# Kernel optimization log

Measured on AMD Instinct MI355X. Metric: run time of the kernel, lower is better.

The kernel has to match this reference:

```python
import jax, jax.numpy as jnp
import numpy as np

D, NH, K, FF, S, B = 256, 4, 1024, 1024, 2048, 4  # nhead*d_model must equal key_feature_dim=1024


def _ln(x, g, b, eps=1e-5):
    m = jnp.mean(x, axis=-1, keepdims=True)
    v = jnp.mean((x - m) ** 2, axis=-1, keepdims=True)
    return (x - m) / jnp.sqrt(v + eps) * g + b


def _l2norm(x, eps=1e-12):  # F.normalize(p=2, dim=-1)
    n = jnp.sqrt(jnp.sum(x * x, axis=-1, keepdims=True))
    return x / jnp.maximum(n, eps)


def setup_inputs() -> dict:
    key = jax.random.key(0)
    ks = jax.random.split(key, 16)
    def rn(i, shape, s):
        return jax.random.normal(ks[i], shape, jnp.float32) * jnp.float32(s)
    z = lambda shape: jnp.zeros(shape, jnp.float32)
    o = lambda shape: jnp.ones(shape, jnp.float32)
    return {
        "srcc": jax.random.normal(ks[0], (S, B, D), jnp.float32),
        "memory": jax.random.normal(ks[1], (S, B, D), jnp.float32),
        # per-head RelationUnit weights (stacked over NH heads)
        "WK": rn(2, (NH, K, D), np.sqrt(2.0 / K)),
        "WQ": rn(3, (NH, K, D), np.sqrt(2.0 / K)),
        "WV": rn(4, (NH, D, D), np.sqrt(2.0 / D)),
        "Wt": rn(5, (NH, D, D), np.sqrt(1.0 / D)),   # trans_conv
        # per-head TransNonlinear (extra_nonlinear)
        "e1w": rn(6, (NH, K, D), np.sqrt(1.0 / D)), "e1b": z((NH, K)),
        "e2w": rn(7, (NH, D, K), np.sqrt(1.0 / K)), "e2b": z((NH, D)),
        "eg": o((NH, D)), "eb": z((NH, D)),
        "Wout": rn(8, (D, NH * D), np.sqrt(1.0 / (NH * D))),  # trans_conv_out
        # decoder-layer FFN + norms
        "l1w": rn(9, (FF, D), np.sqrt(1.0 / D)), "l1b": z((FF,)),
        "l2w": rn(10, (D, FF), np.sqrt(1.0 / FF)), "l2b": z((D,)),
        "n1g": o((D,)), "n1b": z((D,)),
        "n3g": o((D,)), "n3b": z((D,)),
    }


def _forward(srcc, memory, WK, WQ, WV, Wt, e1w, e1b, e2w, e2b, eg, eb,
             Wout, l1w, l1b, l2w, l2b, n1g, n1b, n3g, n3b):
    # RMA(query=memory, key=srcc, value=srcc); dropout = identity (eval mode)
    q, kv = memory, srcc  # [S,B,D]
    wk = _l2norm(jnp.einsum('sbd,hkd->hsbk', kv, WK))   # [h,S,B,K]
    wq = _l2norm(jnp.einsum('sbd,hkd->hsbk', q, WQ))
    dot = jnp.einsum('hqbk,hsbk->hbqs', wq, wk)          # [h,B,Sq,Sk]
    aff = jax.nn.softmax(dot, axis=-1)
    # custom renormalization over the *query* axis (torch dim=1 of [B,Sq,Sk])
    aff = aff / (1e-9 + jnp.sum(aff, axis=2, keepdims=True))
    wv = jnp.einsum('sbd,hed->hbse', kv, WV)             # [h,B,Sk,D]
    o = jnp.einsum('hbqs,hbse->hqbe', aff, wv)           # [h,Sq,B,D]
    ru = jax.nn.relu(jnp.einsum('hqbd,hed->hqbe', q[None] - o, Wt))
    # per-head TransNonlinear
    hmid = jax.nn.relu(jnp.einsum('hqbd,hkd->hqbk', ru, e1w) + e1b[:, None, None, :])
    s2 = jnp.einsum('hqbk,hdk->hqbd', hmid, e2w) + e2b[:, None, None, :]
    xh = _ln(ru + s2, eg[:, None, None, :], eb[:, None, None, :])  # [h,S,B,D]
    cat = jnp.moveaxis(xh, 0, 2).reshape(q.shape[0], q.shape[1], NH * D)  # concat heads
    rma_out = jnp.einsum('sbk,dk->sbd', cat, Wout)       # [S,B,D]
    # decoder layer: note the faithful `[0]` indexing from the source
    srcc2 = rma_out[0]                                    # [B,D]
    x = _ln(memory + srcc2[None, :, :], n1g, n1b)         # broadcast residual
    ff = jax.nn.relu(x @ l1w.T + l1b) @ l2w.T + l2b
    return _ln(x + ff, n3g, n3b)


def reference(srcc, memory, WK, WQ, WV, Wt, e1w, e1b, e2w, e2b, eg, eb,
              Wout, l1w, l1b, l2w, l2b, n1g, n1b, n3g, n3b):
    return _forward(srcc, memory, WK, WQ, WV, Wt, e1w, e1b, e2w, e2b, eg, eb,
                    Wout, l1w, l1b, l2w, l2b, n1g, n1b, n3g, n3b)
```

## Files before the change

### kernel.cpp

```cpp
#include <hip/hip_runtime.h>
#include <stdint.h>
#include <stdio.h>

#define S_  2048
#define B_  4
#define D_  256
#define NH_ 4
#define K_  1024
#define FF_ 1024
#define M_  (S_*B_)
#define HB_ (NH_*B_)

#define LDSROW 136
#define PROW 144

typedef float  f32x4  __attribute__((ext_vector_type(4)));
typedef __bf16 bf16x8 __attribute__((ext_vector_type(8)));

__device__ __forceinline__ float bf2f(unsigned short u) {
  union { unsigned int i; float f; } v; v.i = ((unsigned int)u) << 16; return v.f;
}
__device__ __forceinline__ unsigned short f2bf(float f) {
  union { float f; unsigned int i; } v; v.f = f;
  unsigned int r = v.i + 0x7fffu + ((v.i >> 16) & 1u);
  return (unsigned short)(r >> 16);
}
__device__ __forceinline__ unsigned char f2fp8(float f) {
  return (unsigned char)(__builtin_amdgcn_cvt_pk_fp8_f32(f, f, 0, false) & 0xff);
}

__device__ __forceinline__ void gld_lds16(const void* g, void* l) {
  __builtin_amdgcn_global_load_lds(
      (__attribute__((address_space(1))) void*)(uintptr_t)g,
      (__attribute__((address_space(3))) void*)(uintptr_t)l, 16, 0, 0);
}

__device__ __forceinline__ void gemm_kloop(
    const unsigned short* __restrict__ Ag, const unsigned short* __restrict__ Bg,
    int lda, int ldb, int kdim,
    unsigned short* __restrict__ smA, unsigned short* __restrict__ smB,
    f32x4 acc[4][4])
{
  const int t    = threadIdx.x;
  const int wave = t >> 6;
  const int lane = t & 63;
  const int wm   = (wave >> 1) << 6;
  const int wn   = (wave & 1) << 6;
  const int c16  = lane & 15;
  const int quad = lane >> 4;

  for (int kc = 0; kc < kdim; kc += 64) {
    __syncthreads();
#pragma unroll
    for (int it = 0; it < 4; ++it) {
      int c   = it*256 + t;
      int row = c >> 3;
      int g   = (c & 7) ^ (row & 7);
      const unsigned short* ga = Ag + (size_t)row*lda + kc + g*8;
      const unsigned short* gb = Bg + (size_t)row*ldb + kc + g*8;
      unsigned short* la = smA + (size_t)(it*256 + wave*64)*8;
      unsigned short* lb = smB + (size_t)(it*256 + wave*64)*8;
      gld_lds16(ga, la);
      gld_lds16(gb, lb);
    }
    asm volatile("s_waitcnt vmcnt(0)" ::: "memory");
    __syncthreads();
#pragma unroll
    for (int ks = 0; ks < 2; ++ks) {
      bf16x8 av[4], bv[4];
#pragma unroll
      for (int i = 0; i < 4; ++i) {
        int ra = wm + i*16 + c16;
        av[i] = *(const bf16x8*)(smA + ra*64 + (((ks*4 + quad) ^ (ra & 7)))*8);
        int rb = wn + i*16 + c16;
        bv[i] = *(const bf16x8*)(smB + rb*64 + (((ks*4 + quad) ^ (rb & 7)))*8);
      }
#pragma unroll
      for (int i = 0; i < 4; ++i)
#pragma unroll
        for (int j = 0; j < 4; ++j)
          acc[i][j] = __builtin_amdgcn_mfma_f32_16x16x32_bf16(av[i], bv[j], acc[i][j], 0, 0, 0);
    }
  }
}

__device__ __forceinline__ float blk_sum256(float v, float* red) {
#pragma unroll
  for (int o = 32; o; o >>= 1) v += __shfl_xor(v, o, 64);
  __syncthreads();
  if ((threadIdx.x & 63) == 0) red[threadIdx.x >> 6] = v;
  __syncthreads();
  return red[0] + red[1] + red[2] + red[3];
}

__device__ __forceinline__ float wave_red(float a) {
#pragma unroll
  for (int o = 1; o < 64; o <<= 1) a += __shfl_xor(a, o, 64);
  return a;
}

__global__ void __launch_bounds__(256) k_cvt6(
    const float* __restrict__ s0, unsigned short* __restrict__ d0,
    const float* __restrict__ s1, unsigned short* __restrict__ d1,
    const float* __restrict__ s2, unsigned short* __restrict__ d2,
    const float* __restrict__ s3, unsigned short* __restrict__ d3,
    const float* __restrict__ s4, unsigned short* __restrict__ d4,
    const float* __restrict__ s5, unsigned short* __restrict__ d5) {
  int b = blockIdx.x;
  const float* src; unsigned short* dst; int base;
  if      (b < 2048) { src = s0; dst = d0; base = b; }
  else if (b < 4096) { src = s1; dst = d1; base = b - 2048; }
  else if (b < 5120) { src = s2; dst = d2; base = b - 4096; }
  else if (b < 6144) { src = s3; dst = d3; base = b - 5120; }
  else if (b < 6400) { src = s4; dst = d4; base = b - 6144; }
  else               { src = s5; dst = d5; base = b - 6400; }
  int i = (base*256 + threadIdx.x)*4;
  float4 v = *(const float4*)(src + i);
  ushort4 o;
  o.x = f2bf(v.x); o.y = f2bf(v.y); o.z = f2bf(v.z); o.w = f2bf(v.w);
  *(ushort4*)(dst + i) = o;
}

__global__ void __launch_bounds__(256) k_proj(const unsigned short* __restrict__ X,
    const unsigned short* __restrict__ W, float* __restrict__ nsq,
    unsigned char* __restrict__ outp) {
  __shared__ __align__(16) unsigned short sm[128*LDSROW];
  int l = blockIdx.x, x = l & 7, rblk = l >> 3;
  int m0 = (rblk >> 2)*128;
  int n0 = (x*4 + (rblk & 3))*128;
  f32x4 acc[4][4];
#pragma unroll
  for (int i = 0; i < 4; ++i)
#pragma unroll
    for (int j = 0; j < 4; ++j) acc[i][j] = f32x4{0.f,0.f,0.f,0.f};
  gemm_kloop(X + (size_t)m0*D_, W + (size_t)n0*D_, D_, D_, D_, sm, sm + 128*64, acc);
  const int t = threadIdx.x, wave = t>>6, lane = t&63;
  const int wm = (wave>>1)*64, wn = (wave&1)*64, quad = lane>>4, c16 = lane&15;
  const int h = n0 >> 10;
  unsigned char* sm8 = (unsigned char*)sm;
  __syncthreads();
#pragma unroll
  for (int i = 0; i < 4; ++i)
#pragma unroll
    for (int r = 0; r < 4; ++r) {
      int mloc = wm + i*16 + quad*4 + r;
      float sq = 0.f;
#pragma unroll
      for (int j = 0; j < 4; ++j) {
        float v = acc[i][j][r];
        sm8[mloc*PROW + wn + j*16 + c16] = f2fp8(v);
        sq += v*v;
      }
      sq += __shfl_xor(sq, 1, 64); sq += __shfl_xor(sq, 2, 64);
      sq += __shfl_xor(sq, 4, 64); sq += __shfl_xor(sq, 8, 64);
      if (c16 == 0) {
        int m = m0 + mloc;
        atomicAdd(&nsq[(size_t)(h*B_ + (m & 3))*S_ + (m >> 2)], sq);
      }
    }
  __syncthreads();
  const int cg = t & 7, rsub = t >> 3;
#pragma unroll
  for (int c = 0; c < 4; ++c) {
    int mloc = c*32 + rsub;
    int m = m0 + mloc, s = m >> 2, b = m & 3;
    uint4 val = *(const uint4*)(sm8 + mloc*PROW + cg*16);
    *(uint4*)(outp + ((size_t)(h*B_ + b)*S_ + s)*K_ + (n0 & (K_-1)) + cg*16) = val;
  }
}

__global__ void __launch_bounds__(256) k_qkA(const unsigned char* __restrict__ wqa,
    const unsigned char* __restrict__ wka, const float* __restrict__ nq,
    const float* __restrict__ nk, float* __restrict__ lrow,
    unsigned short* __restrict__ E) {
  __shared__ __align__(16) unsigned short sm[128*LDSROW];
  unsigned char* smA = (unsigned char*)sm;
  unsigned char* smB = smA + 128*128;
  int l = blockIdx.x, x = l & 7, rblk = l >> 3;
  int hb = rblk >> 5;
  int rr = rblk & 31;
  int q0 = (x*2 + (rr & 1))*128;
  int s0 = (rr >> 1)*128;
  const unsigned char* A  = wqa + (size_t)hb*S_*K_ + (size_t)q0*K_;
  const unsigned char* Bm = wka + (size_t)hb*S_*K_ + (size_t)s0*K_;
  const int t = threadIdx.x, wave = t>>6, lane = t&63;
  const int wm = (wave>>1)*64, wn = (wave&1)*64, quad = lane>>4, c16 = lane&15;
  f32x4 acc[4][4];
#pragma unroll
  for (int i = 0; i < 4; ++i)
#pragma unroll
    for (int j = 0; j < 4; ++j) acc[i][j] = f32x4{0.f,0.f,0.f,0.f};

  for (int kc = 0; kc < K_; kc += 128) {
    __syncthreads();
#pragma unroll
    for (int it = 0; it < 4; ++it) {
      int c   = it*256 + t;
      int row = c >> 3;
      int g   = (c & 7) ^ (row & 7);
      gld_lds16(A  + (size_t)row*K_ + kc + g*16, smA + (size_t)(it*256 + wave*64)*16);
      gld_lds16(Bm + (size_t)row*K_ + kc + g*16, smB + (size_t)(it*256 + wave*64)*16);
    }
    asm volatile("s_waitcnt vmcnt(0)" ::: "memory");
    __syncthreads();
#pragma unroll
    for (int ks = 0; ks < 4; ++ks) {
      long av[4], bv[4];
#pragma unroll
      for (int i = 0; i < 4; ++i) {
        int ra = wm + i*16 + c16;
        av[i] = *(const long*)(smA + ra*128 + (((2*ks + (quad>>1)) ^ (ra & 7)))*16 + (quad&1)*8);
        int rb = wn + i*16 + c16;
        bv[i] = *(const long*)(smB + rb*128 + (((2*ks + (quad>>1)) ^ (rb & 7)))*16 + (quad&1)*8);
      }
#pragma unroll
      for (int i = 0; i < 4; ++i)
#pragma unroll
        for (int j = 0; j < 4; ++j)
          acc[i][j] = __builtin_amdgcn_mfma_f32_16x16x32_fp8_fp8(av[i], bv[j], acc[i][j], 0, 0, 0);
    }
  }

  float rk4[4];
#pragma unroll
  for (int j = 0; j < 4; ++j)
    rk4[j] = rsqrtf(nk[(size_t)hb*S_ + s0 + wn + j*16 + c16]);
  __syncthreads();
#pragma unroll
  for (int i = 0; i < 4; ++i)
#pragma unroll
    for (int r = 0; r < 4; ++r) {
      int qloc = wm + i*16 + quad*4 + r;
      float rq = rsqrtf(nq[(size_t)hb*S_ + q0 + qloc]);
      float rs = 0.f;
#pragma unroll
      for (int j = 0; j < 4; ++j) {
        float e = __expf(acc[i][j][r] * rq * rk4[j]);
        rs += e;
        sm[qloc*LDSROW + wn + j*16 + c16] = f2bf(e);
      }
      rs += __shfl_xor(rs, 1, 64); rs += __shfl_xor(rs, 2, 64);
      rs += __shfl_xor(rs, 4, 64); rs += __shfl_xor(rs, 8, 64);
      if (c16 == 0) atomicAdd(&lrow[(size_t)hb*S_ + q0 + qloc], rs);
    }
  __syncthreads();
  const int col8 = (t & 15)*8, rsub = t >> 4;
#pragma unroll
  for (int c = 0; c < 8; ++c) {
    int qloc = c*16 + rsub;
    uint4 val = *(const uint4*)(sm + qloc*LDSROW + col8);
    *(uint4*)(E + ((size_t)hb*S_ + q0 + qloc)*S_ + s0 + col8) = val;
  }
}

__global__ void __launch_bounds__(256) k_colsumE(const unsigned short* __restrict__ E,
    const float* __restrict__ lrow, float* __restrict__ colsum,
    float* __restrict__ p0) {
  __shared__ float il[128];
  int hb = blockIdx.x, qc = blockIdx.y;
  int t  = threadIdx.x;
  if (t < 128) il[t] = 1.f / lrow[(size_t)hb*S_ + qc*128 + t];
  __syncthreads();
  const unsigned short* Eb = E + (size_t)hb*S_*S_ + (size_t)(qc*128)*S_ + t*8;
  float acc8[8] = {0,0,0,0,0,0,0,0};
  for (int qi = 0; qi < 128; ++qi) {
    uint4 u = *(const uint4*)(Eb + (size_t)qi*S_);
    float w = il[qi];
    unsigned int ws_[4] = {u.x, u.y, u.z, u.w};
    float v8[8];
#pragma unroll
    for (int k = 0; k < 4; ++k) {
      v8[2*k]   = bf2f((unsigned short)(ws_[k] & 0xffffu));
      v8[2*k+1] = bf2f((unsigned short)(ws_[k] >> 16));
    }
#pragma unroll
    for (int k = 0; k < 8; ++k) acc8[k] += v8[k] * w;
    if (qc == 0 && qi == 0) {
#pragma unroll
      for (int k = 0; k < 8; ++k) p0[(size_t)hb*S_ + t*8 + k] = v8[k] * w;
    }
  }
#pragma unroll
  for (int k = 0; k < 8; ++k)
    atomicAdd(&colsum[(size_t)hb*S_ + t*8 + k], acc8[k]);
}

__global__ void __launch_bounds__(256) k_mid0(const float* __restrict__ p0,
    const float* __restrict__ colsum, const float* __restrict__ kv,
    float* __restrict__ cbuf) {
  __shared__ float aff[128];
  int hb = blockIdx.x, sc = blockIdx.y;
  int b = hb & 3;
  int t = threadIdx.x;
  if (t < 128) {
    int s = sc*128 + t;
    aff[t] = p0[(size_t)hb*S_ + s] / (1e-9f + colsum[(size_t)hb*S_ + s]);
  }
  __syncthreads();
  float acc = 0.f;
#pragma unroll 4
  for (int i = 0; i < 128; ++i) {
    int s = sc*128 + i;
    acc += aff[i] * kv[((size_t)s*B_ + b)*D_ + t];
  }
  atomicAdd(&cbuf[hb*D_ + t], acc);
}

__global__ void __launch_bounds__(256) k_mid1a(const float* __restrict__ cbuf,
    const float* __restrict__ mem, const float* __restrict__ WV,
    const float* __restrict__ Wt, float* __restrict__ ruW) {
  __shared__ float cS[D_], qmo[D_];
  int hb = blockIdx.x, h = hb >> 2, b = hb & 3;
  int t = threadIdx.x, wave = t >> 6, lane = t & 63;
  cS[t] = cbuf[hb*D_ + t];
  __syncthreads();
  float4 cv = *(const float4*)(cS + lane*4);
  for (int rr = 0; rr < 64; ++rr) {
    int e = wave*64 + rr;
    float4 w = *(const float4*)(WV + ((size_t)h*D_ + e)*D_ + lane*4);
    float a = wave_red(cv.x*w.x + cv.y*w.y + cv.z*w.z + cv.w*w.w);
    if (lane == 0) qmo[e] = mem[(size_t)b*D_ + e] - a;
  }
  __syncthreads();
  float4 qv = *(const float4*)(qmo + lane*4);
  for (int rr = 0; rr < 64; ++rr) {
    int e = wave*64 + rr;
    float4 w = *(const float4*)(Wt + ((size_t)h*D_ + e)*D_ + lane*4);
    float a = wave_red(qv.x*w.x + qv.y*w.y + qv.z*w.z + qv.w*w.w);
    if (lane == 0) ruW[hb*D_ + e] = fmaxf(a, 0.f);
  }
}

__global__ void __launch_bounds__(256) k_mid1b(const float* __restrict__ ruW,
    const float* __restrict__ e1w, const float* __restrict__ e1b,
    float* __restrict__ hmW) {
  __shared__ float ru[D_];
  int hb = blockIdx.x, kc = blockIdx.y, h = hb >> 2;
  int t = threadIdx.x, wave = t >> 6, lane = t & 63;
  ru[t] = ruW[hb*D_ + t];
  __syncthreads();
  float4 rv = *(const float4*)(ru + lane*4);
  for (int rr = 0; rr < 32; ++rr) {
    int k = kc*128 + wave*32 + rr;
    float4 w = *(const float4*)(e1w + ((size_t)h*K_ + k)*D_ + lane*4);
    float a = wave_red(rv.x*w.x + rv.y*w.y + rv.z*w.z + rv.w*w.w);
    if (lane == 0) hmW[hb*K_ + k] = fmaxf(a + e1b[(size_t)h*K_ + k], 0.f);
  }
}

__global__ void __launch_bounds__(256) k_mid1c(const float* __restrict__ hmW,
    const float* __restrict__ e2w, const float* __restrict__ e2b,
    float* __restrict__ s2W) {
  __shared__ float hm[K_];
  int hb = blockIdx.x, dc = blockIdx.y, h = hb >> 2;
  int t = threadIdx.x, wave = t >> 6, lane = t & 63;
  for (int k = t; k < K_; k += 256) hm[k] = hmW[hb*K_ + k];
  __syncthreads();
  for (int rr = 0; rr < 32; ++rr) {
    int d = dc*128 + wave*32 + rr;
    const float* row = e2w + ((size_t)h*D_ + d)*K_;
    float a = 0.f;
#pragma unroll
    for (int p = 0; p < 4; ++p) {
      float4 w = *(const float4*)(row + (p*64 + lane)*4);
      float4 hv = *(const float4*)(hm + (p*64 + lane)*4);
      a += w.x*hv.x + w.y*hv.y + w.z*hv.z + w.w*hv.w;
    }
    a = wave_red(a);
    if (lane == 0) s2W[hb*D_ + d] = a + e2b[(size_t)h*D_ + d];
  }
}

__global__ void __launch_bounds__(256) k_mid1d(const float* __restrict__ ruW,
    const float* __restrict__ s2W, const float* __restrict__ eg,
    const float* __restrict__ ebias, float* __restrict__ xh0) {
  __shared__ float red[4];
  int hb = blockIdx.x, h = hb >> 2;
  int t = threadIdx.x;
  float tv = ruW[hb*D_ + t] + s2W[hb*D_ + t];
  float mean = blk_sum256(tv, red) * (1.f/D_);
  float dv = tv - mean;
  float var = blk_sum256(dv*dv, red) * (1.f/D_);
  xh0[hb*D_ + t] = dv * rsqrtf(var + 1e-5f) * eg[(size_t)h*D_ + t] + ebias[(size_t)h*D_ + t];
}

__global__ void __launch_bounds__(256) k_mid2(const float* __restrict__ xh0,
    const float* __restrict__ Wout, float* __restrict__ srcc2) {
  __shared__ float cat[NH_*D_];
  int b = blockIdx.x, dc = blockIdx.y;
  int t = threadIdx.x, wave = t >> 6, lane = t & 63;
  for (int n = t; n < NH_*D_; n += 256)
    cat[n] = xh0[((size_t)(n >> 8)*B_ + b)*D_ + (n & 255)];
  __syncthreads();
  for (int rr = 0; rr < 32; ++rr) {
    int d = dc*128 + wave*32 + rr;
    const float* row = Wout + (size_t)d*(NH_*D_);
    float a = 0.f;
#pragma unroll
    for (int p = 0; p < 4; ++p) {
      float4 w = *(const float4*)(row + (p*64 + lane)*4);
      float4 cv = *(const float4*)(cat + (p*64 + lane)*4);
      a += w.x*cv.x + w.y*cv.y + w.z*cv.z + w.w*cv.w;
    }
    a = wave_red(a);
    if (lane == 0) srcc2[b*D_ + d] = a;
  }
}

__global__ void __launch_bounds__(256) k_f1(const float* __restrict__ mem,
    const float* __restrict__ srcc2, const float* __restrict__ g,
    const float* __restrict__ bb, float* __restrict__ xf,
    unsigned short* __restrict__ xb) {
  __shared__ float red[4];
  int m = blockIdx.x, t = threadIdx.x;
  float v = mem[(size_t)m*D_ + t] + srcc2[(m & 3)*D_ + t];
  float mean = blk_sum256(v, red) * (1.f/D_);
  float d = v - mean;
  float var = blk_sum256(d*d, red) * (1.f/D_);
  float y = d * rsqrtf(var + 1e-5f) * g[t] + bb[t];
  xf[(size_t)m*D_ + t] = y;
  xb[(size_t)m*D_ + t] = f2bf(y);
}

__global__ void __launch_bounds__(256) k_f2(const unsigned short* __restrict__ xb,
    const unsigned short* __restrict__ l1wb, const float* __restrict__ l1b,
    unsigned short* __restrict__ h1) {
  __shared__ __align__(16) unsigned short sm[128*LDSROW];
  int l = blockIdx.x;
  int n0 = (l & 7)*128, m0 = (l >> 3)*128;
  f32x4 acc[4][4];
#pragma unroll
  for (int i = 0; i < 4; ++i)
#pragma unroll
    for (int j = 0; j < 4; ++j) acc[i][j] = f32x4{0.f,0.f,0.f,0.f};
  gemm_kloop(xb + (size_t)m0*D_, l1wb + (size_t)n0*D_, D_, D_, D_, sm, sm + 128*64, acc);
  const int t = threadIdx.x, wave = t>>6, lane = t&63;
  const int wm = (wave>>1)*64, wn = (wave&1)*64, quad = lane>>4, c16 = lane&15;
  __syncthreads();
#pragma unroll
  for (int i = 0; i < 4; ++i)
#pragma unroll
    for (int r = 0; r < 4; ++r) {
      int mloc = wm + i*16 + quad*4 + r;
#pragma unroll
      for (int j = 0; j < 4; ++j) {
        int n = n0 + wn + j*16 + c16;
        sm[mloc*LDSROW + wn + j*16 + c16] = f2bf(fmaxf(acc[i][j][r] + l1b[n], 0.f));
      }
    }
  __syncthreads();
  const int col8 = (t & 15)*8, rsub = t >> 4;
#pragma unroll
  for (int c = 0; c < 8; ++c) {
    int mloc = c*16 + rsub;
    uint4 val = *(const uint4*)(sm + mloc*LDSROW + col8);
    *(uint4*)(h1 + (size_t)(m0 + mloc)*FF_ + n0 + col8) = val;
  }
}

__global__ void __launch_bounds__(256) k_f3(const unsigned short* __restrict__ h1,
    const unsigned short* __restrict__ l2wb, float* __restrict__ yf) {
  __shared__ __align__(16) unsigned short smA[128*64], smB[128*64];
  int l = blockIdx.x;
  int z = l & 1, n0 = ((l >> 1) & 1)*128, m0 = (l >> 2)*128;
  f32x4 acc[4][4];
#pragma unroll
  for (int i = 0; i < 4; ++i)
#pragma unroll
    for (int j = 0; j < 4; ++j) acc[i][j] = f32x4{0.f,0.f,0.f,0.f};
  gemm_kloop(h1 + (size_t)m0*FF_ + z*512, l2wb + (size_t)n0*FF_ + z*512,
             FF_, FF_, 512, smA, smB, acc);
  const int t = threadIdx.x, wave = t>>6, lane = t&63;
  const int wm = (wave>>1)*64, wn = (wave&1)*64, quad = lane>>4, c16 = lane&15;
#pragma unroll
  for (int i = 0; i < 4; ++i)
#pragma unroll
    for (int r = 0; r < 4; ++r) {
      int m = m0 + wm + i*16 + quad*4 + r;
#pragma unroll
      for (int j = 0; j < 4; ++j) {
        int n = n0 + wn + j*16 + c16;
        atomicAdd(&yf[(size_t)m*D_ + n], acc[i][j][r]);
      }
    }
}

__global__ void __launch_bounds__(256) k_f4(const float* __restrict__ yf,
    const float* __restrict__ l2b, const float* __restrict__ xf,
    const float* __restrict__ g, const float* __restrict__ bb,
    float* __restrict__ out) {
  __shared__ float red[4];
  int m = blockIdx.x, t = threadIdx.x;
  float v = yf[(size_t)m*D_ + t] + l2b[t] + xf[(size_t)m*D_ + t];
  float mean = blk_sum256(v, red) * (1.f/D_);
  float d = v - mean;
  float var = blk_sum256(d*d, red) * (1.f/D_);
  out[(size_t)m*D_ + t] = d * rsqrtf(var + 1e-5f) * g[t] + bb[t];
}

constexpr size_t SZ_ACT  = (size_t)HB_*S_*K_;
constexpr size_t OFF_WQA = 0;
constexpr size_t OFF_WKA = OFF_WQA + SZ_ACT;
constexpr size_t OFF_KVB = OFF_WKA + SZ_ACT;
constexpr size_t OFF_QB  = OFF_KVB + (size_t)M_*D_*2;
constexpr size_t OFF_WKW = OFF_QB  + (size_t)M_*D_*2;
constexpr size_t OFF_WQW = OFF_WKW + (size_t)NH_*K_*D_*2;
constexpr size_t OFF_L1W = OFF_WQW + (size_t)NH_*K_*D_*2;
constexpr size_t OFF_L2W = OFF_L1W + (size_t)FF_*D_*2;
constexpr size_t OFF_XB  = OFF_L2W + (size_t)D_*FF_*2;
constexpr size_t OFF_H1  = OFF_XB  + (size_t)M_*D_*2;
constexpr size_t OFF_XF  = OFF_H1  + (size_t)M_*FF_*2;
constexpr size_t OFF_YF  = OFF_XF  + (size_t)M_*D_*4;
constexpr size_t OFF_NQ  = OFF_YF  + (size_t)M_*D_*4;
constexpr size_t OFF_NK  = OFF_NQ + (size_t)HB_*S_*4;
constexpr size_t OFF_L   = OFF_NK + (size_t)HB_*S_*4;
constexpr size_t OFF_CS  = OFF_L  + (size_t)HB_*S_*4;
constexpr size_t OFF_CB  = OFF_CS + (size_t)HB_*S_*4;
constexpr size_t ZERO_BYTES = (size_t)HB_*S_*4*4 + (size_t)HB_*D_*4;
constexpr size_t OFF_P0  = OFF_CB + (size_t)HB_*D_*4;
constexpr size_t OFF_XH0 = OFF_P0 + (size_t)HB_*S_*4;
constexpr size_t OFF_SC2 = OFF_XH0 + (size_t)HB_*D_*4;
constexpr size_t OFF_RU  = OFF_SC2 + (size_t)B_*D_*4;
constexpr size_t OFF_HM  = OFF_RU  + (size_t)HB_*D_*4;
constexpr size_t OFF_S2  = OFF_HM  + (size_t)HB_*K_*4;
constexpr size_t OFF_E   = OFF_S2  + (size_t)HB_*D_*4;
constexpr size_t SZ_E    = (size_t)HB_*S_*S_*2;
constexpr size_t NEED_ALL = OFF_E + SZ_E;

extern "C" void kernel_launch(void* const* d_in, const int* in_sizes, int n_in,
                              void* d_out, int out_size, void* d_ws, size_t ws_size,
                              hipStream_t stream) {
  (void)in_sizes; (void)out_size;
  if (n_in < 21) return;
  const float* srcc = (const float*)d_in[0];
  const float* mem  = (const float*)d_in[1];
  const float* WK   = (const float*)d_in[2];
  const float* WQ   = (const float*)d_in[3];
  const float* WV   = (const float*)d_in[4];
  const float* Wt   = (const float*)d_in[5];
  const float* e1w  = (const float*)d_in[6];
  const float* e1b  = (const float*)d_in[7];
  const float* e2w  = (const float*)d_in[8];
  const float* e2b  = (const float*)d_in[9];
  const float* eg   = (const float*)d_in[10];
  const float* eb   = (const float*)d_in[11];
  const float* Wout = (const float*)d_in[12];
  const float* l1w  = (const float*)d_in[13];
  const float* l1b  = (const float*)d_in[14];
  const float* l2w  = (const float*)d_in[15];
  const float* l2b  = (const float*)d_in[16];
  const float* n1g  = (const float*)d_in[17];
  const float* n1b  = (const float*)d_in[18];
  const float* n3g  = (const float*)d_in[19];
  const float* n3b  = (const float*)d_in[20];

  char* ws = (char*)d_ws;
  if (ws_size < NEED_ALL) {
    fprintf(stderr, "kernel_launch: ws_size=%zu < required %zu bytes — aborting\n",
            ws_size, NEED_ALL);
    return;
  }

  unsigned char*  wqa  = (unsigned char*)(ws + OFF_WQA);
  unsigned char*  wka  = (unsigned char*)(ws + OFF_WKA);
  unsigned short* kvb  = (unsigned short*)(ws + OFF_KVB);
  unsigned short* qb   = (unsigned short*)(ws + OFF_QB);
  unsigned short* wkw  = (unsigned short*)(ws + OFF_WKW);
  unsigned short* wqw  = (unsigned short*)(ws + OFF_WQW);
  unsigned short* l1wb = (unsigned short*)(ws + OFF_L1W);
  unsigned short* l2wb = (unsigned short*)(ws + OFF_L2W);
  unsigned short* xb   = (unsigned short*)(ws + OFF_XB);
  unsigned short* h1   = (unsigned short*)(ws + OFF_H1);
  float* xf    = (float*)(ws + OFF_XF);
  float* yf    = (float*)(ws + OFF_YF);
  float* nq    = (float*)(ws + OFF_NQ);
  float* nk    = (float*)(ws + OFF_NK);
  float* lrow  = (float*)(ws + OFF_L);
  float* cs    = (float*)(ws + OFF_CS);
  float* cbuf  = (float*)(ws + OFF_CB);
  float* p0    = (float*)(ws + OFF_P0);
  float* xh0   = (float*)(ws + OFF_XH0);
  float* sc2   = (float*)(ws + OFF_SC2);
  float* ruW   = (float*)(ws + OFF_RU);
  float* hmW   = (float*)(ws + OFF_HM);
  float* s2W   = (float*)(ws + OFF_S2);
  unsigned short* E = (unsigned short*)(ws + OFF_E);

  hipMemsetAsync(ws + OFF_NQ, 0, ZERO_BYTES, stream);
  hipMemsetAsync(ws + OFF_YF, 0, (size_t)M_*D_*4, stream);

  k_cvt6<<<6656, 256, 0, stream>>>(srcc, kvb, mem, qb, WK, wkw, WQ, wqw,
                                   l1w, l1wb, l2w, l2wb);

  k_proj<<<2048, 256, 0, stream>>>(kvb, wkw, nk, wka);
  k_proj<<<2048, 256, 0, stream>>>(qb,  wqw, nq, wqa);

  k_qkA<<<4096, 256, 0, stream>>>(wqa, wka, nq, nk, lrow, E);
  k_colsumE<<<dim3(HB_, 16), 256, 0, stream>>>(E, lrow, cs, p0);

  k_mid0<<<dim3(HB_, S_/128), 256, 0, stream>>>(p0, cs, srcc, cbuf);
  k_mid1a<<<HB_, 256, 0, stream>>>(cbuf, mem, WV, Wt, ruW);
  k_mid1b<<<dim3(HB_, 8), 256, 0, stream>>>(ruW, e1w, e1b, hmW);
  k_mid1c<<<dim3(HB_, 2), 256, 0, stream>>>(hmW, e2w, e2b, s2W);
  k_mid1d<<<HB_, 256, 0, stream>>>(ruW, s2W, eg, eb, xh0);
  k_mid2<<<dim3(B_, 2), 256, 0, stream>>>(xh0, Wout, sc2);

  k_f1<<<M_, 256, 0, stream>>>(mem, sc2, n1g, n1b, xf, xb);
  k_f2<<<512, 256, 0, stream>>>(xb, l1wb, l1b, h1);
  k_f3<<<256, 256, 0, stream>>>(h1, l2wb, yf);
  k_f4<<<M_, 256, 0, stream>>>(yf, l2b, xf, n3g, n3b, (float*)d_out);
}
```

Baseline: 700.1 us.

## Use MX fp8 scaled MFMA in QK kernel, merge projections, widen small GEMV grids

The QK affinity kernel now feeds each 128-deep chunk to one mfma_scale 16x16x128 fp8 instruction with unit scales, replacing four 16x16x32 fp8 MFMAs. This cuts the MFMA instruction count and issues wider LDS reads. The two projection launches are merged into one 4096-block kernel that picks its operands by block index, removing a launch and letting both projections fill the GPU together. The mid-stage GEMV kernels k_mid1c and k_mid2 get four times more blocks with fewer rows each, to use more CUs. The LDS read swizzle pattern changes with the new operand layout, which risks bank conflicts or correctness if the layout does not match what the instruction expects.

```diff
diff --git a/kernel.cpp b/kernel.cpp
--- a/kernel.cpp
+++ b/kernel.cpp
@@ -16,6 +16,7 @@
 
 typedef float  f32x4  __attribute__((ext_vector_type(4)));
 typedef __bf16 bf16x8 __attribute__((ext_vector_type(8)));
+typedef int    i32x8  __attribute__((ext_vector_type(8)));
 
 __device__ __forceinline__ float bf2f(unsigned short u) {
   union { unsigned int i; float f; } v; v.i = ((unsigned int)u) << 16; return v.f;
@@ -121,11 +122,18 @@
   *(ushort4*)(dst + i) = o;
 }
 
-__global__ void __launch_bounds__(256) k_proj(const unsigned short* __restrict__ X,
-    const unsigned short* __restrict__ W, float* __restrict__ nsq,
-    unsigned char* __restrict__ outp) {
+__global__ void __launch_bounds__(256) k_proj2(
+    const unsigned short* __restrict__ X0, const unsigned short* __restrict__ W0,
+    float* __restrict__ n0p, unsigned char* __restrict__ o0p,
+    const unsigned short* __restrict__ X1, const unsigned short* __restrict__ W1,
+    float* __restrict__ n1p, unsigned char* __restrict__ o1p) {
   __shared__ __align__(16) unsigned short sm[128*LDSROW];
-  int l = blockIdx.x, x = l & 7, rblk = l >> 3;
+  int which = blockIdx.x >> 11;
+  const unsigned short* X = which ? X1 : X0;
+  const unsigned short* W = which ? W1 : W0;
+  float* nsq = which ? n1p : n0p;
+  unsigned char* outp = which ? o1p : o0p;
+  int l = blockIdx.x & 2047, x = l & 7, rblk = l >> 3;
   int m0 = (rblk >> 2)*128;
   int n0 = (x*4 + (rblk & 3))*128;
   f32x4 acc[4][4];
@@ -203,22 +211,30 @@
     }
     asm volatile("s_waitcnt vmcnt(0)" ::: "memory");
     __syncthreads();
-#pragma unroll
-    for (int ks = 0; ks < 4; ++ks) {
-      long av[4], bv[4];
-#pragma unroll
-      for (int i = 0; i < 4; ++i) {
-        int ra = wm + i*16 + c16;
-        av[i] = *(const long*)(smA + ra*128 + (((2*ks + (quad>>1)) ^ (ra & 7)))*16 + (quad&1)*8);
-        int rb = wn + i*16 + c16;
-        bv[i] = *(const long*)(smB + rb*128 + (((2*ks + (quad>>1)) ^ (rb & 7)))*16 + (quad&1)*8);
-      }
-#pragma unroll
-      for (int i = 0; i < 4; ++i)
-#pragma unroll
-        for (int j = 0; j < 4; ++j)
-          acc[i][j] = __builtin_amdgcn_mfma_f32_16x16x32_fp8_fp8(av[i], bv[j], acc[i][j], 0, 0, 0);
-    }
+    i32x8 av[4], bv[4];
+#pragma unroll
+    for (int i = 0; i < 4; ++i) {
+      int ra = wm + i*16 + c16;
+      int sa0 = ((quad*2)     ^ (ra & 7))*16;
+      int sa1 = ((quad*2 + 1) ^ (ra & 7))*16;
+      uint4 lo = *(const uint4*)(smA + ra*128 + sa0);
+      uint4 hi = *(const uint4*)(smA + ra*128 + sa1);
+      av[i] = i32x8{(int)lo.x,(int)lo.y,(int)lo.z,(int)lo.w,
+                    (int)hi.x,(int)hi.y,(int)hi.z,(int)hi.w};
+      int rb = wn + i*16 + c16;
+      int sb0 = ((quad*2)     ^ (rb & 7))*16;
+      int sb1 = ((quad*2 + 1) ^ (rb & 7))*16;
+      uint4 blo = *(const uint4*)(smB + rb*128 + sb0);
+      uint4 bhi = *(const uint4*)(smB + rb*128 + sb1);
+      bv[i] = i32x8{(int)blo.x,(int)blo.y,(int)blo.z,(int)blo.w,
+                    (int)bhi.x,(int)bhi.y,(int)bhi.z,(int)bhi.w};
+    }
+#pragma unroll
+    for (int i = 0; i < 4; ++i)
+#pragma unroll
+      for (int j = 0; j < 4; ++j)
+        acc[i][j] = __builtin_amdgcn_mfma_scale_f32_16x16x128_f8f6f4(
+            av[i], bv[j], acc[i][j], 0, 0, 0, 0x7f7f7f7f, 0, 0x7f7f7f7f);
   }
 
   float rk4[4];
@@ -356,8 +372,8 @@
   int t = threadIdx.x, wave = t >> 6, lane = t & 63;
   for (int k = t; k < K_; k += 256) hm[k] = hmW[hb*K_ + k];
   __syncthreads();
-  for (int rr = 0; rr < 32; ++rr) {
-    int d = dc*128 + wave*32 + rr;
+  for (int rr = 0; rr < 8; ++rr) {
+    int d = dc*32 + wave*8 + rr;
     const float* row = e2w + ((size_t)h*D_ + d)*K_;
     float a = 0.f;
 #pragma unroll
@@ -392,8 +408,8 @@
   for (int n = t; n < NH_*D_; n += 256)
     cat[n] = xh0[((size_t)(n >> 8)*B_ + b)*D_ + (n & 255)];
   __syncthreads();
-  for (int rr = 0; rr < 32; ++rr) {
-    int d = dc*128 + wave*32 + rr;
+  for (int rr = 0; rr < 8; ++rr) {
+    int d = dc*32 + wave*8 + rr;
     const float* row = Wout + (size_t)d*(NH_*D_);
     float a = 0.f;
 #pragma unroll
@@ -592,8 +608,7 @@
   k_cvt6<<<6656, 256, 0, stream>>>(srcc, kvb, mem, qb, WK, wkw, WQ, wqw,
                                    l1w, l1wb, l2w, l2wb);
 
-  k_proj<<<2048, 256, 0, stream>>>(kvb, wkw, nk, wka);
-  k_proj<<<2048, 256, 0, stream>>>(qb,  wqw, nq, wqa);
+  k_proj2<<<4096, 256, 0, stream>>>(kvb, wkw, nk, wka, qb, wqw, nq, wqa);
 
   k_qkA<<<4096, 256, 0, stream>>>(wqa, wka, nq, nk, lrow, E);
   k_colsumE<<<dim3(HB_, 16), 256, 0, stream>>>(E, lrow, cs, p0);
@@ -601,9 +616,9 @@
   k_mid0<<<dim3(HB_, S_/128), 256, 0, stream>>>(p0, cs, srcc, cbuf);
   k_mid1a<<<HB_, 256, 0, stream>>>(cbuf, mem, WV, Wt, ruW);
   k_mid1b<<<dim3(HB_, 8), 256, 0, stream>>>(ruW, e1w, e1b, hmW);
-  k_mid1c<<<dim3(HB_, 2), 256, 0, stream>>>(hmW, e2w, e2b, s2W);
+  k_mid1c<<<dim3(HB_, 8), 256, 0, stream>>>(hmW, e2w, e2b, s2W);
   k_mid1d<<<HB_, 256, 0, stream>>>(ruW, s2W, eg, eb, xh0);
-  k_mid2<<<dim3(B_, 2), 256, 0, stream>>>(xh0, Wout, sc2);
+  k_mid2<<<dim3(B_, 8), 256, 0, stream>>>(xh0, Wout, sc2);
 
   k_f1<<<M_, 256, 0, stream>>>(mem, sc2, n1g, n1b, xf, xb);
   k_f2<<<512, 256, 0, stream>>>(xb, l1wb, l1b, h1);
```

Result: no change. 706.6 us (+0.9%).
